# Kernel tuning notes

Hardware: AMD Instinct MI355X
Metric: run time of the kernel (lower is better)

## Reference

```python
import jax, jax.numpy as jnp
import numpy as np

N, E, G = 100000, 1600000, 64
D, F, FE, LV, OUT = 128, 128, 3, 3, 128
EPS = 1e-5


def setup_inputs() -> dict:
    key = jax.random.key(0)
    ks = jax.random.split(key, 12)
    nrm = lambda k, s, sc: jax.random.normal(k, s, jnp.float32) * sc
    inp = {}
    inp["node_feat"] = nrm(ks[0], (N, F), 1.0)
    inp["edge_feat"] = nrm(ks[1], (E, FE), 1.0)
    inp["edge_from_idx"] = jax.random.randint(ks[2], (E,), 0, N)
    inp["edge_to_idx"] = jax.random.randint(ks[3], (E,), 0, N)
    inp["g_idx"] = jnp.sort(jax.random.randint(ks[4], (N,), 0, G))
    inp["num_graphs"] = G
    sF, sE, sD = 1/np.sqrt(F), 1/np.sqrt(FE), 1/np.sqrt(D)
    inp["w_n2l_w"] = nrm(ks[5], (F, D), sF); inp["w_n2l_b"] = jnp.zeros((D,), jnp.float32)
    inp["w_e2l_w"] = nrm(ks[6], (LV+1, FE, D), sE); inp["w_e2l_b"] = jnp.zeros((LV+1, D), jnp.float32)
    inp["conv_w"] = nrm(ks[7], (LV, D, D), sD); inp["conv_b"] = jnp.zeros((LV, D), jnp.float32)
    inp["l2_w"] = nrm(ks[8], (LV, D, D), sD); inp["l2_b"] = jnp.zeros((LV, D), jnp.float32)
    inp["msg_bn_g"] = jnp.ones((LV+1, D), jnp.float32); inp["msg_bn_b"] = jnp.zeros((LV+1, D), jnp.float32)
    inp["hid_bn_g"] = jnp.ones((LV, D), jnp.float32); inp["hid_bn_b"] = jnp.zeros((LV, D), jnp.float32)
    inp["readout_w"] = nrm(ks[9], (D, OUT), sD); inp["readout_b"] = jnp.zeros((OUT,), jnp.float32)
    return inp


def _bn(x, g, b):
    # BatchNorm1d, training mode (biased batch variance), affine
    m = jnp.mean(x, axis=0)
    v = jnp.var(x, axis=0)
    return g * (x - m) * jax.lax.rsqrt(v + EPS) + b


def reference(node_feat, edge_feat, w_n2l_w, w_n2l_b, w_e2l_w, w_e2l_b,
              conv_w, conv_b, l2_w, l2_b, msg_bn_g, msg_bn_b,
              hid_bn_g, hid_bn_b, readout_w, readout_b,
              edge_from_idx, edge_to_idx, g_idx, num_graphs):
    n_nodes = node_feat.shape[0]
    seg = lambda m: jax.ops.segment_sum(m, edge_to_idx, num_segments=n_nodes)
    # input message: node linear + scatter_add of edge linear
    msg = node_feat @ w_n2l_w + w_n2l_b + seg(edge_feat @ w_e2l_w[0] + w_e2l_b[0])
    h = _bn(jax.nn.relu(msg), msg_bn_g[0], msg_bn_b[0])  # [N, D]
    for lv in range(conv_w.shape[0]):
        # mean-field layer: aggregate neighbor states, then linear update
        node_lin = seg(h[edge_from_idx]) @ conv_w[lv] + conv_b[lv]
        e2n = seg(edge_feat @ w_e2l_w[lv + 1] + w_e2l_b[lv + 1])
        merged = _bn(jax.nn.relu(node_lin + e2n), hid_bn_g[lv], hid_bn_b[lv])
        h = _bn(jax.nn.relu(merged @ l2_w[lv] + l2_b[lv] + h),
                msg_bn_g[lv + 1], msg_bn_b[lv + 1])
    # readout: gnn_out='last', readout_agg='max', act_last=True, bn=False
    gemb = jax.ops.segment_max(h, g_idx, num_segments=num_graphs)  # [G, D]
    return jax.nn.relu(gemb @ readout_w + readout_b)
```

## Files before the change

kernel.cpp:

```cpp
#include <hip/hip_runtime.h>
#include <hip/hip_bf16.h>

#define NN 100000
#define NE 1600000
#define DD 128
#define GG 64
#define BN_EPS 1e-5f
#define NCOPY 16

typedef unsigned short u16;
typedef unsigned char u8;
using f32x4 = __attribute__((ext_vector_type(4))) float;
using f32x2 = __attribute__((ext_vector_type(2))) float;
using s16x8 = __attribute__((ext_vector_type(8))) short;

constexpr int SCAN_B = 1024;
constexpr int NB = (NN + SCAN_B - 1) / SCAN_B;

__device__ __forceinline__ unsigned enc_f(float v) {
  unsigned u = __float_as_uint(v);
  return (u & 0x80000000u) ? ~u : (u | 0x80000000u);
}
__device__ __forceinline__ float dec_f(unsigned k) {
  unsigned u = (k & 0x80000000u) ? (k & 0x7FFFFFFFu) : ~k;
  return __uint_as_float(u);
}
__device__ __forceinline__ u16 f2b(float x) {
  __hip_bfloat16 h = __float2bfloat16(x);
  return *(u16*)&h;
}
__device__ __forceinline__ float b2f(u16 u) {
  unsigned v = ((unsigned)u) << 16;
  return __uint_as_float(v);
}
__device__ __forceinline__ float blo(unsigned v) { return __uint_as_float(v << 16); }
__device__ __forceinline__ float bhi(unsigned v) { return __uint_as_float(v & 0xFFFF0000u); }

__global__ void k_init(int* cursor, float* stats_raw, float* stats_fin,
                       unsigned* gemb_enc) {
  int i = blockIdx.x * blockDim.x + threadIdx.x;
  if (i < NN) cursor[i] = 0;
  if (i < 7 * NCOPY * 256) stats_raw[i] = 0.f;
  if (i < 4 * 256) stats_fin[i] = 0.f;
  if (i < GG*DD) gemb_enc[i] = 0x007FFFFFu;
}

__global__ void k_fill1(const int* __restrict__ to, int* cursor, int* __restrict__ tmp_pos) {
  int e = blockIdx.x * blockDim.x + threadIdx.x;
  if (e >= NE) return;
  tmp_pos[e] = atomicAdd(&cursor[to[e]], 1);
}

__global__ void k_scan1(const int* __restrict__ deg, int* row_ptr, int* bsum) {
  __shared__ int lds[SCAN_B];
  int t = threadIdx.x, i = blockIdx.x * SCAN_B + t;
  int v = (i < NN) ? deg[i] : 0;
  lds[t] = v;
  __syncthreads();
  for (int off = 1; off < SCAN_B; off <<= 1) {
    int add = (t >= off) ? lds[t - off] : 0;
    __syncthreads();
    lds[t] += add;
    __syncthreads();
  }
  if (i < NN) row_ptr[i] = lds[t] - v;
  if (t == SCAN_B - 1) bsum[blockIdx.x] = lds[t];
}

__global__ void k_scan2(const int* __restrict__ bsum, int* boff, int* row_ptr) {
  __shared__ int lds[128];
  int t = threadIdx.x;
  int v = (t < NB) ? bsum[t] : 0;
  lds[t] = v;
  __syncthreads();
  for (int off = 1; off < 128; off <<= 1) {
    int add = (t >= off) ? lds[t - off] : 0;
    __syncthreads();
    lds[t] += add;
    __syncthreads();
  }
  if (t < NB) boff[t] = lds[t] - v;
  if (t == 127) row_ptr[NN] = lds[127];
}

__global__ void k_scan3(int* row_ptr, const int* __restrict__ boff) {
  int i = blockIdx.x * blockDim.x + threadIdx.x;
  if (i >= NN) return;
  row_ptr[i] += boff[i >> 10];
}

__global__ void k_fill2(const int* __restrict__ from, const int* __restrict__ to,
                        const int* __restrict__ tmp_pos, const int* __restrict__ row_ptr,
                        uint2* __restrict__ csr2) {
  int e = blockIdx.x * blockDim.x + threadIdx.x;
  if (e >= NE) return;
  int pos = row_ptr[to[e]] + tmp_pos[e];
  csr2[pos] = make_uint2((unsigned)from[e], (unsigned)e);
}

__global__ void k_node_ef(const float* __restrict__ ef, const int* __restrict__ row_ptr,
                          const uint2* __restrict__ csr2, float* __restrict__ agg4) {
  int grp = (blockIdx.x * 256 + threadIdx.x) >> 4;
  if (grp >= NN) return;
  int l = threadIdx.x & 15;
  int s = row_ptr[grp], e = row_ptr[grp + 1];
  float a0 = 0.f, a1 = 0.f, a2 = 0.f;
  for (int i = s + l; i < e; i += 16) {
    int eid = (int)csr2[i].y;
    a0 += ef[(size_t)eid * 3 + 0];
    a1 += ef[(size_t)eid * 3 + 1];
    a2 += ef[(size_t)eid * 3 + 2];
  }
#pragma unroll
  for (int off = 8; off; off >>= 1) {
    a0 += __shfl_down(a0, off, 16);
    a1 += __shfl_down(a1, off, 16);
    a2 += __shfl_down(a2, off, 16);
  }
  if (l == 0)
    ((float4*)agg4)[grp] = make_float4(a0, a1, a2, (float)(e - s));
}

__global__ void k_redstat(const float* __restrict__ raw, float* __restrict__ fin) {
  int c = threadIdx.x;
  float s = 0.f;
#pragma unroll
  for (int i = 0; i < NCOPY; ++i) s += raw[i * 256 + c];
  fin[c] = s;
}

__global__ __launch_bounds__(256)
void k_gather(const u8* __restrict__ R8, u16* __restrict__ out,
              const int* __restrict__ row_ptr, const uint2* __restrict__ csr2,
              const float* __restrict__ stats, const float* __restrict__ g,
              const float* __restrict__ b) {
  const int wid = (blockIdx.x * 256 + threadIdx.x) >> 6;
  if (wid >= NN) return;
  const int lane = threadIdx.x & 63;
  const int esel = lane >> 4;
  const int dpos = lane & 15;
  const int s = row_ptr[wid], e = row_ptr[wid + 1];
  const uint2* R2 = (const uint2*)R8;
  f32x2 a01 = {0.f, 0.f}, a23 = {0.f, 0.f}, a45 = {0.f, 0.f}, a67 = {0.f, 0.f};
#define ACC(V)                                                        \
  a01 += __builtin_amdgcn_cvt_pk_f32_fp8((int)V.x, false);            \
  a23 += __builtin_amdgcn_cvt_pk_f32_fp8((int)V.x, true);             \
  a45 += __builtin_amdgcn_cvt_pk_f32_fp8((int)V.y, false);            \
  a67 += __builtin_amdgcn_cvt_pk_f32_fp8((int)V.y, true);
  int i = s;
  for (; i + 15 < e; i += 16) {
    int q0 = (int)csr2[i      + esel].x;
    int q1 = (int)csr2[i + 4  + esel].x;
    int q2 = (int)csr2[i + 8  + esel].x;
    int q3 = (int)csr2[i + 12 + esel].x;
    uint2 w0 = R2[(size_t)q0 * 16 + dpos];
    uint2 w1 = R2[(size_t)q1 * 16 + dpos];
    uint2 w2 = R2[(size_t)q2 * 16 + dpos];
    uint2 w3 = R2[(size_t)q3 * 16 + dpos];
    ACC(w0) ACC(w1) ACC(w2) ACC(w3)
  }
  for (; i + 3 < e; i += 4) {
    int q = (int)csr2[i + esel].x;
    uint2 wv = R2[(size_t)q * 16 + dpos];
    ACC(wv)
  }
  if (i < e && esel < e - i) {
    int q = (int)csr2[i + esel].x;
    uint2 wv = R2[(size_t)q * 16 + dpos];
    ACC(wv)
  }
#undef ACC
  float a[8] = {a01.x, a01.y, a23.x, a23.y, a45.x, a45.y, a67.x, a67.y};
#pragma unroll
  for (int j = 0; j < 8; ++j) {
    a[j] += __shfl_xor(a[j], 16);
    a[j] += __shfl_xor(a[j], 32);
  }
  if (esel == 0) {
    const int d0 = dpos * 8;
    float dg = (float)(e - s);
    unsigned pk[4];
#pragma unroll
    for (int h = 0; h < 4; ++h) {
      float r[2];
#pragma unroll
      for (int j = 0; j < 2; ++j) {
        int d = d0 + h * 2 + j;
        float m  = stats[d] * (1.f / NN);
        float vv = stats[DD + d] * (1.f / NN) - m * m;
        float sc = g[d] * rsqrtf(vv + BN_EPS);
        float sh = b[d] - m * sc;
        r[j] = sc * a[h * 2 + j] + sh * dg;
      }
      pk[h] = (unsigned)f2b(r[0]) | ((unsigned)f2b(r[1]) << 16);
    }
    uint4 v; v.x = pk[0]; v.y = pk[1]; v.z = pk[2]; v.w = pk[3];
    ((uint4*)out)[(size_t)wid * 16 + dpos] = v;
  }
}

template<int MODE>
__device__ __forceinline__ void wprep_body(
    const float* __restrict__ W, const float* __restrict__ bias,
    const float* __restrict__ in_stats, const float* __restrict__ in_g,
    const float* __restrict__ in_b,
    const float* __restrict__ res_stats, const float* __restrict__ res_g,
    const float* __restrict__ res_b,
    u16* __restrict__ WT, float* __restrict__ biasP, float* __restrict__ rese) {
  __shared__ float s_s[DD], s_t[DD];
  int t = threadIdx.x;
  if (t < DD) {
    float s = 1.f, tt = 0.f;
    if (MODE == 1) {
      float s1 = 0.f, s2 = 0.f, r1 = 0.f, r2 = 0.f;
#pragma unroll
      for (int i = 0; i < NCOPY; ++i) {
        s1 += in_stats[i * 256 + t];
        s2 += in_stats[i * 256 + DD + t];
        r1 += res_stats[i * 256 + t];
        r2 += res_stats[i * 256 + DD + t];
      }
      float mean = s1 * (1.f / NN);
      float var  = s2 * (1.f / NN) - mean * mean;
      float rs = rsqrtf(var + BN_EPS);
      s = in_g[t] * rs;
      tt = in_b[t] - mean * s;
      float m2 = r1 * (1.f / NN);
      float v2 = r2 * (1.f / NN) - m2 * m2;
      float rr = rsqrtf(v2 + BN_EPS);
      float sc = res_g[t] * rr;
      rese[t] = sc;
      rese[DD + t] = res_b[t] - m2 * sc;
    }
    s_s[t] = s; s_t[t] = tt;
  }
  __syncthreads();
  for (int idx = t; idx < DD * DD; idx += 256) {
    int k = idx >> 7, n = idx & 127;
    WT[n * DD + k] = f2b(W[idx] * s_s[k]);
  }
  if (t < DD) {
    float acc = bias[t];
    if (MODE == 1)
      for (int k = 0; k < DD; ++k) acc += s_t[k] * W[k * DD + t];
    biasP[t] = acc;
  }
}

__global__ void k_wprep0(const float* __restrict__ w_n2l_w, const float* __restrict__ w_n2l_b,
                         const float* __restrict__ conv_w, const float* __restrict__ conv_b,
                         u16* wt0, float* bp0, u16* wt1, float* bp1,
                         u16* wt3, float* bp3, u16* wt5, float* bp5) {
  int blk = blockIdx.x;
  const float* W; const float* bias; u16* WT; float* biasP;
  if (blk == 0)      { W = w_n2l_w;              bias = w_n2l_b;          WT = wt0; biasP = bp0; }
  else if (blk == 1) { W = conv_w;               bias = conv_b;           WT = wt1; biasP = bp1; }
  else if (blk == 2) { W = conv_w + DD * DD;     bias = conv_b + DD;      WT = wt3; biasP = bp3; }
  else               { W = conv_w + 2 * DD * DD; bias = conv_b + 2 * DD;  WT = wt5; biasP = bp5; }
  wprep_body<0>(W, bias, nullptr, nullptr, nullptr, nullptr, nullptr, nullptr,
                WT, biasP, nullptr);
}

__global__ void k_wprep1(const float* __restrict__ W, const float* __restrict__ bias,
                         const float* __restrict__ in_stats, const float* __restrict__ in_g,
                         const float* __restrict__ in_b,
                         const float* __restrict__ res_stats, const float* __restrict__ res_g,
                         const float* __restrict__ res_b,
                         u16* WT, float* biasP, float* rese) {
  wprep_body<1>(W, bias, in_stats, in_g, in_b, res_stats, res_g, res_b, WT, biasP, rese);
}

__device__ __forceinline__ int swz_addr(int row_bytes, int xr, int g, int o) {
  return row_bytes + ((((g & 7) ^ xr) | (g & 8)) << 4) + o;
}

template<int MODE>
__global__ __launch_bounds__(256, 2)
void k_gemm(const void* __restrict__ Ain, const u16* __restrict__ WT,
            const float* __restrict__ biasP, u16* __restrict__ out,
            u8* __restrict__ out8,
            float* __restrict__ stats_out,
            const float* __restrict__ rese, const u16* __restrict__ resid,
            const float4* __restrict__ agg4,
            const float* __restrict__ w_e2l, const float* __restrict__ b_e2l) {
  __shared__ __align__(16) u16 lds_a[128 * 128];
  __shared__ __align__(16) u16 lds_b[128 * 128];
  __shared__ float sstats[256];
  const int tid  = threadIdx.x;
  const int lane = tid & 63;
  const int wv   = tid >> 6;
  const int row0 = blockIdx.x * 128;

  sstats[tid] = 0.f;

#pragma unroll
  for (int c = 0; c < 8; ++c) {
    int gidx = (wv * 8 + c) * 64 + lane;
    int row = gidx >> 4, gL = gidx & 15;
    int gS = (gL & 8) | ((gL & 7) ^ (row & 7));
    const u16* gsrcB = WT + (size_t)row * DD + gS * 8;
    u16* ldstB = lds_b + (size_t)(wv * 8 + c) * 512;
    __builtin_amdgcn_global_load_lds(
        (const __attribute__((address_space(1))) unsigned int*)gsrcB,
        (__attribute__((address_space(3))) unsigned int*)ldstB, 16, 0, 0);
    if (MODE != 2) {
      int arow = row0 + row; if (arow >= NN) arow = NN - 1;
      const u16* gsrcA = (const u16*)Ain + (size_t)arow * DD + gS * 8;
      u16* ldstA = lds_a + (size_t)(wv * 8 + c) * 512;
      __builtin_amdgcn_global_load_lds(
          (const __attribute__((address_space(1))) unsigned int*)gsrcA,
          (__attribute__((address_space(3))) unsigned int*)ldstA, 16, 0, 0);
    }
  }
  if (MODE == 2) {
    const float2* Af = (const float2*)Ain;
#pragma unroll
    for (int k = 0; k < 32; ++k) {
      int idx = k * 256 + tid;
      int r = idx >> 6, ln = idx & 63;
      int n = row0 + r; if (n >= NN) n = NN - 1;
      float2 v = Af[(size_t)n * 64 + ln];
      unsigned pk = (unsigned)f2b(v.x) | ((unsigned)f2b(v.y) << 16);
      int gLn = ln >> 2, oin = (ln & 3) * 4;
      int gS = (gLn & 8) | ((gLn & 7) ^ (r & 7));
      *(unsigned*)((char*)lds_a + r * 256 + gS * 16 + oin) = pk;
    }
  }
  __syncthreads();

  const int colid = lane & 15;
  const int lgrp  = lane >> 4;
  const int rowbase = wv * 32;
  const int o = (lgrp & 1) * 8;

  s16x8 afr[2][4];
#pragma unroll
  for (int rf = 0; rf < 2; ++rf) {
    int r = rowbase + rf * 16 + colid;
    int rb = r << 8, xr = r & 7;
#pragma unroll
    for (int ks = 0; ks < 4; ++ks) {
      int g0 = ks * 4 + (lgrp >> 1);
      uint2 lo = *(const uint2*)((const char*)lds_a + swz_addr(rb, xr, g0, o));
      uint2 hi = *(const uint2*)((const char*)lds_a + swz_addr(rb, xr, g0 + 2, o));
      union { unsigned u[4]; s16x8 v; } pk;
      pk.u[0] = lo.x; pk.u[1] = lo.y; pk.u[2] = hi.x; pk.u[3] = hi.y;
      afr[rf][ks] = pk.v;
    }
  }

  s16x8 aext[2];
  if (MODE != 1) {
#pragma unroll
    for (int rf = 0; rf < 2; ++rf) {
      int r = row0 + rowbase + rf * 16 + colid;
      if (r >= NN) r = NN - 1;
      float4 a4 = agg4[r];
      union { unsigned u[4]; s16x8 v; } pk;
      pk.u[0] = (lgrp == 0) ? ((unsigned)f2b(a4.x) | ((unsigned)f2b(a4.y) << 16)) : 0u;
      pk.u[1] = (lgrp == 0) ? ((unsigned)f2b(a4.z) | ((unsigned)f2b(a4.w) << 16)) : 0u;
      pk.u[2] = 0u; pk.u[3] = 0u;
      aext[rf] = pk.v;
    }
  }
  __syncthreads();

  if (MODE == 1) {
#pragma unroll
    for (int c = 0; c < 8; ++c) {
      int gidx = (wv * 8 + c) * 64 + lane;
      int row = gidx >> 4, gL = gidx & 15;
      int gS = (gL & 8) | ((gL & 7) ^ (row & 7));
      int arow = row0 + row; if (arow >= NN) arow = NN - 1;
      const u16* gsrcR = resid + (size_t)arow * DD + gS * 8;
      u16* ldstR = lds_a + (size_t)(wv * 8 + c) * 512;
      __builtin_amdgcn_global_load_lds(
          (const __attribute__((address_space(1))) unsigned int*)gsrcR,
          (__attribute__((address_space(3))) unsigned int*)ldstR, 16, 0, 0);
    }
  }

  f32x4 acc[2][8];
#pragma unroll
  for (int cf = 0; cf < 8; ++cf) {
    const int col = cf * 16 + colid;
    const float bp = biasP[col];
    acc[0][cf] = (f32x4){bp, bp, bp, bp};
    acc[1][cf] = (f32x4){bp, bp, bp, bp};
    int nb = col << 8, xn = col & 7;
#pragma unroll
    for (int ks = 0; ks < 4; ++ks) {
      int g0 = ks * 4 + (lgrp >> 1);
      uint2 lo = *(const uint2*)((const char*)lds_b + swz_addr(nb, xn, g0, o));
      uint2 hi = *(const uint2*)((const char*)lds_b + swz_addr(nb, xn, g0 + 2, o));
      union { unsigned u[4]; s16x8 v; } pk;
      pk.u[0] = lo.x; pk.u[1] = lo.y; pk.u[2] = hi.x; pk.u[3] = hi.y;
      acc[0][cf] = __builtin_amdgcn_mfma_f32_16x16x32_bf16(afr[0][ks], pk.v, acc[0][cf], 0, 0, 0);
      acc[1][cf] = __builtin_amdgcn_mfma_f32_16x16x32_bf16(afr[1][ks], pk.v, acc[1][cf], 0, 0, 0);
    }
    if (MODE != 1) {
      union { unsigned u[4]; s16x8 v; } bx;
      if (lgrp == 0) {
        float w0 = w_e2l[col], w1 = w_e2l[DD + col];
        float w2 = w_e2l[2 * DD + col], be = b_e2l[col];
        bx.u[0] = (unsigned)f2b(w0) | ((unsigned)f2b(w1) << 16);
        bx.u[1] = (unsigned)f2b(w2) | ((unsigned)f2b(be) << 16);
      } else { bx.u[0] = 0u; bx.u[1] = 0u; }
      bx.u[2] = 0u; bx.u[3] = 0u;
      acc[0][cf] = __builtin_amdgcn_mfma_f32_16x16x32_bf16(aext[0], bx.v, acc[0][cf], 0, 0, 0);
      acc[1][cf] = __builtin_amdgcn_mfma_f32_16x16x32_bf16(aext[1], bx.v, acc[1][cf], 0, 0, 0);
    }
  }
  __syncthreads();

#pragma unroll
  for (int cf = 0; cf < 8; ++cf) {
    const int col = cf * 16 + colid;
    float sc, sh;
    if (MODE == 1) { sc = rese[col]; sh = rese[DD + col]; }
    float s = 0.f, s2 = 0.f;
    int gc = col >> 3, cb = (col & 7) * 2;
#pragma unroll
    for (int rf = 0; rf < 2; ++rf)
#pragma unroll
      for (int q = 0; q < 4; ++q) {
        int rloc = rowbase + rf * 16 + lgrp * 4 + q;
        int r = row0 + rloc;
        float v = acc[rf][cf][q];
        if (MODE == 1) {
          int gsr = (gc & 8) | ((gc & 7) ^ (rloc & 7));
          u16 rv = *(const u16*)((const char*)lds_a + rloc * 256 + gsr * 16 + cb);
          v += sc * b2f(rv) + sh;
        }
        v = fmaxf(v, 0.f);
        if (r < NN) { s += v; s2 += v * v; }
        int gso = (gc & 8) | ((gc & 7) ^ (rloc & 7));
        *(u16*)((char*)lds_b + rloc * 256 + gso * 16 + cb) = f2b(v);
      }
    s  += __shfl_xor(s, 16);  s  += __shfl_xor(s, 32);
    s2 += __shfl_xor(s2, 16); s2 += __shfl_xor(s2, 32);
    if (lgrp == 0) {
      atomicAdd(&sstats[col], s);
      atomicAdd(&sstats[DD + col], s2);
    }
  }
  __syncthreads();

#pragma unroll
  for (int k = 0; k < 8; ++k) {
    int idx = k * 256 + tid;
    int r = idx >> 4, g = idx & 15;
    if (row0 + r < NN) {
      int gd = (g & 8) | ((g & 7) ^ (r & 7));
      uint4 v = *(const uint4*)((const char*)lds_b + r * 256 + g * 16);
      *(uint4*)(out + (size_t)(row0 + r) * DD + gd * 8) = v;
      if (MODE != 0) {
        int p0 = 0, p1 = 0;
        p0 = __builtin_amdgcn_cvt_pk_fp8_f32(blo(v.x), bhi(v.x), p0, false);
        p0 = __builtin_amdgcn_cvt_pk_fp8_f32(blo(v.y), bhi(v.y), p0, true);
        p1 = __builtin_amdgcn_cvt_pk_fp8_f32(blo(v.z), bhi(v.z), p1, false);
        p1 = __builtin_amdgcn_cvt_pk_fp8_f32(blo(v.w), bhi(v.w), p1, true);
        uint2 o8; o8.x = (unsigned)p0; o8.y = (unsigned)p1;
        *(uint2*)(out8 + (size_t)(row0 + r) * DD + gd * 8) = o8;
      }
    }
  }
  atomicAdd(&stats_out[(blockIdx.x & (NCOPY - 1)) * 256 + tid], sstats[tid]);
}

__global__ void k_segmax(const u16* __restrict__ R, const int* __restrict__ g_idx,
                         unsigned* __restrict__ gemb_enc,
                         const float* __restrict__ stats, const float* __restrict__ g,
                         const float* __restrict__ b) {
  int t = blockIdx.x * blockDim.x + threadIdx.x;
  int d = t & (DD - 1);
  int chunk = t >> 7;
  int n0 = chunk * 8;
  if (n0 >= NN) return;
  float mean = stats[d] * (1.f / NN);
  float var  = stats[DD + d] * (1.f / NN) - mean * mean;
  float rs = rsqrtf(var + BN_EPS);
  float scale = g[d] * rs;
  float shift = b[d] - mean * scale;
  int cur = -1; float run = 0.f;
  int nend = n0 + 8; if (nend > NN) nend = NN;
  for (int n = n0; n < nend; ++n) {
    float v = scale * b2f(R[(size_t)n * DD + d]) + shift;
    int gi = g_idx[n];
    if (gi != cur) {
      if (cur >= 0) atomicMax(&gemb_enc[cur * DD + d], enc_f(run));
      cur = gi; run = v;
    } else {
      run = fmaxf(run, v);
    }
  }
  if (cur >= 0) atomicMax(&gemb_enc[cur * DD + d], enc_f(run));
}

__global__ void k_readout(const unsigned* __restrict__ gemb,
                          const float* __restrict__ W, const float* __restrict__ b,
                          float* __restrict__ out) {
  __shared__ float row[DD];
  int g = blockIdx.x, t = threadIdx.x;
  row[t] = dec_f(gemb[g * DD + t]);
  __syncthreads();
  float acc = b[t];
  for (int d = 0; d < DD; ++d) acc += row[d] * W[d * DD + t];
  out[g * DD + t] = fmaxf(acc, 0.f);
}

extern "C" void kernel_launch(void* const* d_in, const int* in_sizes, int n_in,
                              void* d_out, int out_size, void* d_ws, size_t ws_size,
                              hipStream_t stream) {
  const float* node_feat = (const float*)d_in[0];
  const float* edge_feat = (const float*)d_in[1];
  const int*   efrom     = (const int*)d_in[2];
  const int*   eto       = (const int*)d_in[3];
  const int*   g_idx     = (const int*)d_in[4];
  const float* w_n2l_w   = (const float*)d_in[6];
  const float* w_n2l_b   = (const float*)d_in[7];
  const float* w_e2l_w   = (const float*)d_in[8];
  const float* w_e2l_b   = (const float*)d_in[9];
  const float* conv_w    = (const float*)d_in[10];
  const float* conv_b    = (const float*)d_in[11];
  const float* l2_w      = (const float*)d_in[12];
  const float* l2_b      = (const float*)d_in[13];
  const float* msg_bn_g  = (const float*)d_in[14];
  const float* msg_bn_b  = (const float*)d_in[15];
  const float* hid_bn_g  = (const float*)d_in[16];
  const float* hid_bn_b  = (const float*)d_in[17];
  const float* readout_w = (const float*)d_in[18];
  const float* readout_b = (const float*)d_in[19];
  float* out = (float*)d_out;
  (void)in_sizes; (void)n_in; (void)out_size; (void)ws_size;

  char* ws = (char*)d_ws;
  size_t off = 0;
  auto alloc = [&](size_t bytes) -> void* {
    void* p = ws + off; off += (bytes + 511) & ~(size_t)511; return p;
  };
  u16*      Pb0     = (u16*)alloc((size_t)NN * DD * 2);
  u16*      Pb1     = (u16*)alloc((size_t)NN * DD * 2);
  u16*      Pb2     = (u16*)alloc((size_t)NN * DD * 2);
  u8*       P8a     = (u8*)alloc((size_t)NN * DD);
  u8*       P8b     = (u8*)alloc((size_t)NN * DD);
  float*    agg4    = (float*)alloc((size_t)NN * 4 * 4);
  int*      cursor  = (int*)alloc((size_t)NN * 4);
  int*      row_ptr = (int*)alloc((size_t)(NN + 1) * 4);
  int*      tmp_pos = (int*)alloc((size_t)NE * 4);
  uint2*    csr2    = (uint2*)alloc((size_t)NE * 8);
  int*      bsum    = (int*)alloc((size_t)NB * 4);
  int*      boff    = (int*)alloc((size_t)NB * 4);
  float*    stats   = (float*)alloc((size_t)7 * NCOPY * 256 * 4);
  float*    statfin = (float*)alloc((size_t)4 * 256 * 4);
  unsigned* gemb    = (unsigned*)alloc((size_t)GG * DD * 4);
  u16*      wt[7];
  float*    bp[7];
  float*    re[7];
  for (int i = 0; i < 7; ++i) {
    wt[i] = (u16*)alloc((size_t)DD * DD * 2);
    bp[i] = (float*)alloc((size_t)DD * 4);
    re[i] = (float*)alloc((size_t)2 * DD * 4);
  }

  k_init<<<(NN + 255) / 256, 256, 0, stream>>>(cursor, stats, statfin, gemb);
  k_fill1<<<(NE + 255) / 256, 256, 0, stream>>>(eto, cursor, tmp_pos);
  k_scan1<<<NB, SCAN_B, 0, stream>>>(cursor, row_ptr, bsum);
  k_scan2<<<1, 128, 0, stream>>>(bsum, boff, row_ptr);
  k_scan3<<<(NN + 255) / 256, 256, 0, stream>>>(row_ptr, boff);
  k_fill2<<<(NE + 255) / 256, 256, 0, stream>>>(efrom, eto, tmp_pos, row_ptr, csr2);
  k_node_ef<<<(NN * 16 + 255) / 256, 256, 0, stream>>>(edge_feat, row_ptr, csr2,
                                                       agg4);
  k_wprep0<<<4, 256, 0, stream>>>(w_n2l_w, w_n2l_b, conv_w, conv_b,
                                  wt[0], bp[0], wt[1], bp[1], wt[3], bp[3], wt[5], bp[5]);

  float* msg_raw[4] = { stats + 0*NCOPY*256, stats + 1*NCOPY*256,
                        stats + 2*NCOPY*256, stats + 3*NCOPY*256 };
  float* hid_raw[3] = { stats + 4*NCOPY*256, stats + 5*NCOPY*256, stats + 6*NCOPY*256 };
  float* msg_fin[4] = { statfin, statfin + 256, statfin + 512, statfin + 768 };
  const int GEMM_GRID = (NN + 127) / 128;

  k_gemm<2><<<GEMM_GRID, 256, 0, stream>>>(node_feat, wt[0], bp[0], Pb0, P8a, msg_raw[0],
      nullptr, nullptr, (const float4*)agg4, w_e2l_w + 0 * 3 * DD, w_e2l_b + 0 * DD);
  k_redstat<<<1, 256, 0, stream>>>(msg_raw[0], msg_fin[0]);

  u16* R = Pb0; u16* other = Pb1;
  u8*  R8 = P8a; u8* other8 = P8b;
  for (int lv = 0; lv < 3; ++lv) {
    int wc = 1 + 2 * lv, wl = 2 + 2 * lv;
    k_gather<<<(NN * 64 + 255) / 256, 256, 0, stream>>>(R8, other, row_ptr, csr2,
        msg_fin[lv], msg_bn_g + lv * DD, msg_bn_b + lv * DD);
    k_gemm<0><<<GEMM_GRID, 256, 0, stream>>>(other, wt[wc], bp[wc], Pb2, nullptr,
        hid_raw[lv], nullptr, nullptr, (const float4*)agg4,
        w_e2l_w + (size_t)(lv + 1) * 3 * DD, w_e2l_b + (lv + 1) * DD);
    k_wprep1<<<1, 256, 0, stream>>>(l2_w + (size_t)lv * DD * DD, l2_b + lv * DD,
        hid_raw[lv], hid_bn_g + lv * DD, hid_bn_b + lv * DD,
        msg_raw[lv], msg_bn_g + lv * DD, msg_bn_b + lv * DD, wt[wl], bp[wl], re[wl]);
    k_gemm<1><<<GEMM_GRID, 256, 0, stream>>>(Pb2, wt[wl], bp[wl], other, other8,
        msg_raw[lv + 1], re[wl], R, nullptr, nullptr, nullptr);
    k_redstat<<<1, 256, 0, stream>>>(msg_raw[lv + 1], msg_fin[lv + 1]);
    u16* t = R; R = other; other = t;
    u8*  t8 = R8; R8 = other8; other8 = t8;
  }

  k_segmax<<<(NN / 8) * DD / 256, 256, 0, stream>>>(
      R, g_idx, gemb, msg_fin[3], msg_bn_g + 3 * DD, msg_bn_b + 3 * DD);
  k_readout<<<GG, DD, 0, stream>>>(gemb, readout_w, readout_b, out);
}
```

Measured before the change: 592.9 us.

## Build CSR with two-pass bucketed counting sort instead of global atomics

```diff
diff --git a/kernel.cpp b/kernel.cpp
--- a/kernel.cpp
+++ b/kernel.cpp
@@ -8,15 +8,17 @@
 #define BN_EPS 1e-5f
 #define NCOPY 16
 
+#define NBKT 128
+#define NPB 782
+#define NBLK_A 400
+#define EPB 4000
+
 typedef unsigned short u16;
 typedef unsigned char u8;
 using f32x4 = __attribute__((ext_vector_type(4))) float;
 using f32x2 = __attribute__((ext_vector_type(2))) float;
 using s16x8 = __attribute__((ext_vector_type(8))) short;
 
-constexpr int SCAN_B = 1024;
-constexpr int NB = (NN + SCAN_B - 1) / SCAN_B;
-
 __device__ __forceinline__ unsigned enc_f(float v) {
   unsigned u = __float_as_uint(v);
   return (u & 0x80000000u) ? ~u : (u | 0x80000000u);
@@ -36,66 +38,129 @@
 __device__ __forceinline__ float blo(unsigned v) { return __uint_as_float(v << 16); }
 __device__ __forceinline__ float bhi(unsigned v) { return __uint_as_float(v & 0xFFFF0000u); }
 
-__global__ void k_init(int* cursor, float* stats_raw, float* stats_fin,
-                       unsigned* gemb_enc) {
+__global__ void k_init(float* stats_raw, float* stats_fin, unsigned* gemb_enc) {
   int i = blockIdx.x * blockDim.x + threadIdx.x;
-  if (i < NN) cursor[i] = 0;
   if (i < 7 * NCOPY * 256) stats_raw[i] = 0.f;
   if (i < 4 * 256) stats_fin[i] = 0.f;
   if (i < GG*DD) gemb_enc[i] = 0x007FFFFFu;
 }
 
-__global__ void k_fill1(const int* __restrict__ to, int* cursor, int* __restrict__ tmp_pos) {
-  int e = blockIdx.x * blockDim.x + threadIdx.x;
-  if (e >= NE) return;
-  tmp_pos[e] = atomicAdd(&cursor[to[e]], 1);
-}
-
-__global__ void k_scan1(const int* __restrict__ deg, int* row_ptr, int* bsum) {
-  __shared__ int lds[SCAN_B];
-  int t = threadIdx.x, i = blockIdx.x * SCAN_B + t;
-  int v = (i < NN) ? deg[i] : 0;
+__global__ void k_histA(const int* __restrict__ to, int* __restrict__ bh) {
+  __shared__ int h[NBKT];
+  int t = threadIdx.x, b = blockIdx.x;
+  if (t < NBKT) h[t] = 0;
+  __syncthreads();
+  int e0 = b * EPB;
+  for (int i = t; i < EPB; i += 256) {
+    int e = e0 + i;
+    if (e < NE) atomicAdd(&h[to[e] / NPB], 1);
+  }
+  __syncthreads();
+  if (t < NBKT) bh[t * NBLK_A + b] = h[t];
+}
+
+__global__ void k_scanA1(int* data, int* bsum) {
+  __shared__ int lds[1024];
+  int t = threadIdx.x, i = blockIdx.x * 1024 + t;
+  int v = data[i];
   lds[t] = v;
   __syncthreads();
-  for (int off = 1; off < SCAN_B; off <<= 1) {
-    int add = (t >= off) ? lds[t - off] : 0;
+  for (int off = 1; off < 1024; off <<= 1) {
+    int a = (t >= off) ? lds[t - off] : 0;
     __syncthreads();
-    lds[t] += add;
+    lds[t] += a;
     __syncthreads();
   }
-  if (i < NN) row_ptr[i] = lds[t] - v;
-  if (t == SCAN_B - 1) bsum[blockIdx.x] = lds[t];
-}
-
-__global__ void k_scan2(const int* __restrict__ bsum, int* boff, int* row_ptr) {
-  __shared__ int lds[128];
+  data[i] = lds[t] - v;
+  if (t == 1023) bsum[blockIdx.x] = lds[t];
+}
+
+__global__ void k_scanA2(const int* __restrict__ bsum, int* boff) {
+  __shared__ int lds[64];
   int t = threadIdx.x;
-  int v = (t < NB) ? bsum[t] : 0;
+  int v = (t < 50) ? bsum[t] : 0;
   lds[t] = v;
   __syncthreads();
-  for (int off = 1; off < 128; off <<= 1) {
-    int add = (t >= off) ? lds[t - off] : 0;
+  for (int off = 1; off < 64; off <<= 1) {
+    int a = (t >= off) ? lds[t - off] : 0;
     __syncthreads();
-    lds[t] += add;
+    lds[t] += a;
     __syncthreads();
   }
-  if (t < NB) boff[t] = lds[t] - v;
-  if (t == 127) row_ptr[NN] = lds[127];
-}
-
-__global__ void k_scan3(int* row_ptr, const int* __restrict__ boff) {
-  int i = blockIdx.x * blockDim.x + threadIdx.x;
-  if (i >= NN) return;
-  row_ptr[i] += boff[i >> 10];
-}
-
-__global__ void k_fill2(const int* __restrict__ from, const int* __restrict__ to,
-                        const int* __restrict__ tmp_pos, const int* __restrict__ row_ptr,
-                        uint2* __restrict__ csr2) {
-  int e = blockIdx.x * blockDim.x + threadIdx.x;
-  if (e >= NE) return;
-  int pos = row_ptr[to[e]] + tmp_pos[e];
-  csr2[pos] = make_uint2((unsigned)from[e], (unsigned)e);
+  if (t < 50) boff[t] = lds[t] - v;
+}
+
+__global__ void k_scanA3(int* data, const int* __restrict__ boff) {
+  int i = blockIdx.x * 1024 + threadIdx.x;
+  data[i] += boff[blockIdx.x];
+}
+
+__global__ void k_scatter1(const int* __restrict__ to, const int* __restrict__ from,
+                           const int* __restrict__ S, int* __restrict__ tmp_dst,
+                           uint2* __restrict__ tmp_se) {
+  __shared__ int cur[NBKT];
+  int t = threadIdx.x, b = blockIdx.x;
+  if (t < NBKT) cur[t] = S[t * NBLK_A + b];
+  __syncthreads();
+  int e0 = b * EPB;
+  for (int i = t; i < EPB; i += 256) {
+    int e = e0 + i;
+    if (e < NE) {
+      int n = to[e];
+      int p = atomicAdd(&cur[n / NPB], 1);
+      tmp_dst[p] = n;
+      tmp_se[p] = make_uint2((unsigned)from[e], (unsigned)e);
+    }
+  }
+}
+
+__global__ __launch_bounds__(256)
+void k_sort2(const int* __restrict__ S, const int* __restrict__ tmp_dst,
+             const uint2* __restrict__ tmp_se, int* __restrict__ row_ptr,
+             uint2* __restrict__ csr2) {
+  __shared__ int hist[NPB];
+  __shared__ int tsum[256];
+  const int k = blockIdx.x, t = threadIdx.x;
+  const int base = k * NPB;
+  const int lo = S[k * NBLK_A];
+  const int hi = (k == NBKT - 1) ? NE : S[(k + 1) * NBLK_A];
+  for (int j = t; j < NPB; j += 256) hist[j] = 0;
+  __syncthreads();
+  for (int i = lo + t; i < hi; i += 256)
+    atomicAdd(&hist[tmp_dst[i] - base], 1);
+  __syncthreads();
+  int j0 = t * 4;
+  int v0 = (j0 + 0 < NPB) ? hist[j0 + 0] : 0;
+  int v1 = (j0 + 1 < NPB) ? hist[j0 + 1] : 0;
+  int v2 = (j0 + 2 < NPB) ? hist[j0 + 2] : 0;
+  int v3 = (j0 + 3 < NPB) ? hist[j0 + 3] : 0;
+  int s = v0 + v1 + v2 + v3;
+  tsum[t] = s;
+  __syncthreads();
+  for (int off = 1; off < 256; off <<= 1) {
+    int a = (t >= off) ? tsum[t - off] : 0;
+    __syncthreads();
+    tsum[t] += a;
+    __syncthreads();
+  }
+  int tb = tsum[t] - s;
+  __syncthreads();
+  int e0 = lo + tb, e1 = e0 + v0, e2 = e1 + v1, e3 = e2 + v2;
+  if (j0 + 0 < NPB) hist[j0 + 0] = e0;
+  if (j0 + 1 < NPB) hist[j0 + 1] = e1;
+  if (j0 + 2 < NPB) hist[j0 + 2] = e2;
+  if (j0 + 3 < NPB) hist[j0 + 3] = e3;
+  if (j0 + 0 < NPB && base + j0 + 0 < NN) row_ptr[base + j0 + 0] = e0;
+  if (j0 + 1 < NPB && base + j0 + 1 < NN) row_ptr[base + j0 + 1] = e1;
+  if (j0 + 2 < NPB && base + j0 + 2 < NN) row_ptr[base + j0 + 2] = e2;
+  if (j0 + 3 < NPB && base + j0 + 3 < NN) row_ptr[base + j0 + 3] = e3;
+  if (k == NBKT - 1 && t == 0) row_ptr[NN] = NE;
+  __syncthreads();
+  for (int i = lo + t; i < hi; i += 256) {
+    int n = tmp_dst[i];
+    int p = atomicAdd(&hist[n - base], 1);
+    csr2[p] = tmp_se[i];
+  }
 }
 
 __global__ void k_node_ef(const float* __restrict__ ef, const int* __restrict__ row_ptr,
@@ -545,12 +610,11 @@
   u8*       P8a     = (u8*)alloc((size_t)NN * DD);
   u8*       P8b     = (u8*)alloc((size_t)NN * DD);
   float*    agg4    = (float*)alloc((size_t)NN * 4 * 4);
-  int*      cursor  = (int*)alloc((size_t)NN * 4);
   int*      row_ptr = (int*)alloc((size_t)(NN + 1) * 4);
-  int*      tmp_pos = (int*)alloc((size_t)NE * 4);
   uint2*    csr2    = (uint2*)alloc((size_t)NE * 8);
-  int*      bsum    = (int*)alloc((size_t)NB * 4);
-  int*      boff    = (int*)alloc((size_t)NB * 4);
+  int*      S       = (int*)alloc((size_t)NBKT * NBLK_A * 4);
+  int*      bsumA   = (int*)alloc((size_t)64 * 4);
+  int*      boffA   = (int*)alloc((size_t)64 * 4);
   float*    stats   = (float*)alloc((size_t)7 * NCOPY * 256 * 4);
   float*    statfin = (float*)alloc((size_t)4 * 256 * 4);
   unsigned* gemb    = (unsigned*)alloc((size_t)GG * DD * 4);
@@ -562,13 +626,16 @@
     bp[i] = (float*)alloc((size_t)DD * 4);
     re[i] = (float*)alloc((size_t)2 * DD * 4);
   }
-
-  k_init<<<(NN + 255) / 256, 256, 0, stream>>>(cursor, stats, statfin, gemb);
-  k_fill1<<<(NE + 255) / 256, 256, 0, stream>>>(eto, cursor, tmp_pos);
-  k_scan1<<<NB, SCAN_B, 0, stream>>>(cursor, row_ptr, bsum);
-  k_scan2<<<1, 128, 0, stream>>>(bsum, boff, row_ptr);
-  k_scan3<<<(NN + 255) / 256, 256, 0, stream>>>(row_ptr, boff);
-  k_fill2<<<(NE + 255) / 256, 256, 0, stream>>>(efrom, eto, tmp_pos, row_ptr, csr2);
+  int*   tmp_dst = (int*)Pb2;
+  uint2* tmp_se  = (uint2*)((char*)Pb2 + (size_t)NE * 4);
+
+  k_init<<<(NN + 255) / 256, 256, 0, stream>>>(stats, statfin, gemb);
+  k_histA<<<NBLK_A, 256, 0, stream>>>(eto, S);
+  k_scanA1<<<50, 1024, 0, stream>>>(S, bsumA);
+  k_scanA2<<<1, 64, 0, stream>>>(bsumA, boffA);
+  k_scanA3<<<50, 1024, 0, stream>>>(S, boffA);
+  k_scatter1<<<NBLK_A, 256, 0, stream>>>(eto, efrom, S, tmp_dst, tmp_se);
+  k_sort2<<<NBKT, 256, 0, stream>>>(S, tmp_dst, tmp_se, row_ptr, csr2);
   k_node_ef<<<(NN * 16 + 255) / 256, 256, 0, stream>>>(edge_feat, row_ptr, csr2,
                                                        agg4);
   k_wprep0<<<4, 256, 0, stream>>>(w_n2l_w, w_n2l_b, conv_w, conv_b,
```

Measured after the change: 573.7 us. 1.03x faster.
